# Kernel optimization log

Measured on AMD Instinct MI355X. Metric: run time of the kernel, lower is better.

## Reference

```python
import jax, jax.numpy as jnp
import numpy as np


def setup_inputs() -> dict:
    key = jax.random.key(0)
    k1, k2 = jax.random.split(key)
    x = jax.random.normal(k1, (8, 64, 224, 224), dtype=jnp.float32)
    kernel = jax.random.normal(k2, (64, 1, 3, 3), dtype=jnp.float32)
    return {"x": x, "kernel": kernel, "stride": 1, "padding": 1, "dilation": 1}


def reference(x, kernel, stride, padding, dilation):
    # Tropical-max (morphological dilation) conv: out[b,c,i,j] =
    #   max_{ki,kj} x_pad[b,c,i*stride+ki*dilation, j*stride+kj*dilation] + kernel[c,0,ki,kj]
    # Padding uses the tropical neutral element -inf, matching the torch module.
    B, C, H, W = x.shape
    O, _, K, _ = kernel.shape
    out_h = (H + 2 * padding - dilation * (K - 1) - 1) // stride + 1
    out_w = (W + 2 * padding - dilation * (K - 1) - 1) // stride + 1
    neutral = -jnp.inf
    xp = jnp.pad(x, ((0, 0), (0, 0), (padding, padding), (padding, padding)),
                 constant_values=neutral)
    # Initialize at -inf: equivalent to the module's extra neutral pad on the K axis.
    acc = jnp.full((B, C, out_h, out_w), neutral, dtype=x.dtype)
    h_span = (out_h - 1) * stride + 1
    w_span = (out_w - 1) * stride + 1
    # Small fixed K*K loop over kernel taps; avoids materializing the unfolded tensor.
    for ki in range(K):
        for kj in range(K):
            patch = jax.lax.slice(
                xp,
                (0, 0, ki * dilation, kj * dilation),
                (B, C, ki * dilation + h_span, kj * dilation + w_span),
                (1, 1, stride, stride),
            )  # [B, C, out_h, out_w]
            acc = jnp.maximum(acc, patch + kernel[None, :, 0, ki, kj, None, None])
    return acc
```

## Files before the change

kernel.cpp:

```cpp
#include <hip/hip_runtime.h>
#include <math.h>


#define H_DIM 224
#define W_DIM 224
#define SR    4
#define SPP   56
#define C_DIM 64
#define NXCD  8

__global__ __launch_bounds__(256) void tropical_conv_kernel(
    const float* __restrict__ x,
    const float* __restrict__ kern,
    float* __restrict__ out)
{
    int bid  = blockIdx.x;
    int cpx  = gridDim.x >> 3;
    int swz  = (bid & (NXCD - 1)) * cpx + (bid >> 3);

    int lane = threadIdx.x & 63;
    int wid  = swz * 4 + (threadIdx.x >> 6);

    int s  = wid % SPP;
    int bc = wid / SPP;
    int c  = bc & (C_DIM - 1);

    const float* kc = kern + c * 9;
    float k00 = kc[0], k01 = kc[1], k02 = kc[2];
    float k10 = kc[3], k11 = kc[4], k12 = kc[5];
    float k20 = kc[6], k21 = kc[7], k22 = kc[8];

    const float NEG = -INFINITY;

    const float* plane  = x   + (size_t)bc * (H_DIM * W_DIM);
    float*       oplane = out + (size_t)bc * (H_DIM * W_DIM);

    int i0  = s * SR;
    int cl  = (lane < 56) ? lane : 55;
    int col = cl * 4;

    float4 rv[SR + 2];
    #pragma unroll
    for (int rr = 0; rr < SR + 2; ++rr) {
        int r  = i0 - 1 + rr;
        int rc = r < 0 ? 0 : (r > H_DIM - 1 ? H_DIM - 1 : r);
        rv[rr] = *(const float4*)(plane + (size_t)rc * W_DIM + col);
    }
    __builtin_amdgcn_sched_barrier(0);

    bool top = (s == 0);
    bool bot = (s == SPP - 1);
    rv[0].x = top ? NEG : rv[0].x;
    rv[0].y = top ? NEG : rv[0].y;
    rv[0].z = top ? NEG : rv[0].z;
    rv[0].w = top ? NEG : rv[0].w;
    rv[SR + 1].x = bot ? NEG : rv[SR + 1].x;
    rv[SR + 1].y = bot ? NEG : rv[SR + 1].y;
    rv[SR + 1].z = bot ? NEG : rv[SR + 1].z;
    rv[SR + 1].w = bot ? NEG : rv[SR + 1].w;

    float lf[SR + 2], rg[SR + 2];
    #pragma unroll
    for (int rr = 0; rr < SR + 2; ++rr) {
        float up = __shfl_up(rv[rr].w, 1);
        float dn = __shfl_down(rv[rr].x, 1);
        lf[rr] = (lane > 0)  ? up : NEG;
        rg[rr] = (lane < 55) ? dn : NEG;
    }

    #pragma unroll
    for (int o = 0; o < SR; ++o) {
        float4 acc = make_float4(NEG, NEG, NEG, NEG);
        #pragma unroll
        for (int ki = 0; ki < 3; ++ki) {
            int rr = o + ki;
            float t0 = (ki == 0) ? k00 : (ki == 1) ? k10 : k20;
            float t1 = (ki == 0) ? k01 : (ki == 1) ? k11 : k21;
            float t2 = (ki == 0) ? k02 : (ki == 1) ? k12 : k22;
            float4 a = rv[rr];
            acc.x = fmaxf(acc.x, fmaxf(fmaxf(lf[rr] + t0, a.x + t1), a.y    + t2));
            acc.y = fmaxf(acc.y, fmaxf(fmaxf(a.x    + t0, a.y + t1), a.z    + t2));
            acc.z = fmaxf(acc.z, fmaxf(fmaxf(a.y    + t0, a.z + t1), a.w    + t2));
            acc.w = fmaxf(acc.w, fmaxf(fmaxf(a.z    + t0, a.w + t1), rg[rr] + t2));
        }
        if (lane < 56) {
            *(float4*)(oplane + (size_t)(i0 + o) * W_DIM + col) = acc;
        }
    }
}

extern "C" void kernel_launch(void* const* d_in, const int* in_sizes, int n_in,
                              void* d_out, int out_size, void* d_ws, size_t ws_size,
                              hipStream_t stream) {
    const float* x    = (const float*)d_in[0];
    const float* kern = (const float*)d_in[1];
    float* out        = (float*)d_out;

    const int grid  = 8 * C_DIM * SPP / 4;
    const int block = 256;
    tropical_conv_kernel<<<grid, block, 0, stream>>>(x, kern, out);
}
```

Measured before the change: 185.9 us.

## Use taller row strips with a rolling 4-row register pipeline

Each wave now processes 16 output rows instead of 4, which cuts the halo-row reload overhead from 6/4 to 18/16 rows read per row written. Input rows are software-pipelined through a 4-slot ring of registers: the next row's load is issued while the current output row is computed, with sched_barriers to keep the order. The grid shrinks to a quarter as many blocks, which lowers parallelism and may expose latency because each wave has fewer loads in flight.

Result: slower. 193.4 us (+4.0%).

```diff
diff --git a/kernel.cpp b/kernel.cpp
--- a/kernel.cpp
+++ b/kernel.cpp
@@ -4,10 +4,9 @@
 
 #define H_DIM 224
 #define W_DIM 224
-#define SR    4
-#define SPP   56
+#define SR    16
+#define SPP   14
 #define C_DIM 64
-#define NXCD  8
 
 __global__ __launch_bounds__(256) void tropical_conv_kernel(
     const float* __restrict__ x,
@@ -16,8 +15,7 @@
 {
     int bid  = blockIdx.x;
     int cpx  = gridDim.x >> 3;
-    int swz  = (bid & (NXCD - 1)) * cpx + (bid >> 3);
-
+    int swz  = (bid & 7) * cpx + (bid >> 3);
     int lane = threadIdx.x & 63;
     int wid  = swz * 4 + (threadIdx.x >> 6);
 
@@ -39,54 +37,62 @@
     int cl  = (lane < 56) ? lane : 55;
     int col = cl * 4;
 
-    float4 rv[SR + 2];
-    #pragma unroll
-    for (int rr = 0; rr < SR + 2; ++rr) {
-        int r  = i0 - 1 + rr;
-        int rc = r < 0 ? 0 : (r > H_DIM - 1 ? H_DIM - 1 : r);
-        rv[rr] = *(const float4*)(plane + (size_t)rc * W_DIM + col);
-    }
+    float4 rv[4];
+    float  lf[4], rg[4];
+
+#define ISSUE(k) do {                                                        \
+        int _r  = i0 - 1 + (k);                                              \
+        int _rc = _r < 0 ? 0 : (_r > H_DIM - 1 ? H_DIM - 1 : _r);            \
+        rv[(k) & 3] = *(const float4*)(plane + (size_t)_rc * W_DIM + col);   \
+    } while (0)
+
+#define ARRIVE(k, dead) do {                                                 \
+        int   _sl = (k) & 3;                                                 \
+        float4 _v = rv[_sl];                                                 \
+        float _up = __shfl_up(_v.w, 1);                                      \
+        float _dn = __shfl_down(_v.x, 1);                                    \
+        bool  _d  = (dead);                                                  \
+        _v.x = _d ? NEG : _v.x;                                              \
+        _v.y = _d ? NEG : _v.y;                                              \
+        _v.z = _d ? NEG : _v.z;                                              \
+        _v.w = _d ? NEG : _v.w;                                              \
+        rv[_sl] = _v;                                                        \
+        lf[_sl] = (_d || lane == 0)  ? NEG : _up;                            \
+        rg[_sl] = (_d || lane >= 55) ? NEG : _dn;                            \
+    } while (0)
+
+    ISSUE(0); ISSUE(1); ISSUE(2);
     __builtin_amdgcn_sched_barrier(0);
-
-    bool top = (s == 0);
-    bool bot = (s == SPP - 1);
-    rv[0].x = top ? NEG : rv[0].x;
-    rv[0].y = top ? NEG : rv[0].y;
-    rv[0].z = top ? NEG : rv[0].z;
-    rv[0].w = top ? NEG : rv[0].w;
-    rv[SR + 1].x = bot ? NEG : rv[SR + 1].x;
-    rv[SR + 1].y = bot ? NEG : rv[SR + 1].y;
-    rv[SR + 1].z = bot ? NEG : rv[SR + 1].z;
-    rv[SR + 1].w = bot ? NEG : rv[SR + 1].w;
-
-    float lf[SR + 2], rg[SR + 2];
-    #pragma unroll
-    for (int rr = 0; rr < SR + 2; ++rr) {
-        float up = __shfl_up(rv[rr].w, 1);
-        float dn = __shfl_down(rv[rr].x, 1);
-        lf[rr] = (lane > 0)  ? up : NEG;
-        rg[rr] = (lane < 55) ? dn : NEG;
-    }
+    ARRIVE(0, s == 0);
+    ARRIVE(1, false);
 
     #pragma unroll
     for (int o = 0; o < SR; ++o) {
+        if (o + 3 <= SR + 1) {
+            ISSUE(o + 3);
+        }
+        __builtin_amdgcn_sched_barrier(0);
+        ARRIVE(o + 2, (s == SPP - 1) && (o + 2 == SR + 1));
+
         float4 acc = make_float4(NEG, NEG, NEG, NEG);
         #pragma unroll
         for (int ki = 0; ki < 3; ++ki) {
-            int rr = o + ki;
+            int sl = (o + ki) & 3;
             float t0 = (ki == 0) ? k00 : (ki == 1) ? k10 : k20;
             float t1 = (ki == 0) ? k01 : (ki == 1) ? k11 : k21;
             float t2 = (ki == 0) ? k02 : (ki == 1) ? k12 : k22;
-            float4 a = rv[rr];
-            acc.x = fmaxf(acc.x, fmaxf(fmaxf(lf[rr] + t0, a.x + t1), a.y    + t2));
+            float4 a = rv[sl];
+            acc.x = fmaxf(acc.x, fmaxf(fmaxf(lf[sl] + t0, a.x + t1), a.y    + t2));
             acc.y = fmaxf(acc.y, fmaxf(fmaxf(a.x    + t0, a.y + t1), a.z    + t2));
             acc.z = fmaxf(acc.z, fmaxf(fmaxf(a.y    + t0, a.z + t1), a.w    + t2));
-            acc.w = fmaxf(acc.w, fmaxf(fmaxf(a.z    + t0, a.w + t1), rg[rr] + t2));
+            acc.w = fmaxf(acc.w, fmaxf(fmaxf(a.z    + t0, a.w + t1), rg[sl] + t2));
         }
         if (lane < 56) {
             *(float4*)(oplane + (size_t)(i0 + o) * W_DIM + col) = acc;
         }
     }
+#undef ISSUE
+#undef ARRIVE
 }
 
 extern "C" void kernel_launch(void* const* d_in, const int* in_sizes, int n_in,
```
